# Optimization experiments

Hardware: AMD Instinct MI355X
Metric: run time of the kernel (lower is better)

Reference implementation:

```python
import jax, jax.numpy as jnp
import numpy as np

B, S, I, H, O = 2048, 128, 1, 512, 1
OUT_SEQ_LEN = 24


def setup_inputs() -> dict:
    key = jax.random.key(0)
    ks = jax.random.split(key, 12)
    s = 1.0 / np.sqrt(H)
    u = lambda k, shape: jax.random.uniform(k, shape, jnp.float32, -s, s)
    return {
        'x': jax.random.normal(ks[0], (B, S, I), jnp.float32),
        'enc_Wih': u(ks[1], (H, I)),
        'enc_Whh': u(ks[2], (H, H)),
        'enc_bih': u(ks[3], (H,)),
        'enc_bhh': u(ks[4], (H,)),
        'dec_Wih': u(ks[5], (H, I)),
        'dec_Whh': u(ks[6], (H, H)),
        'dec_bih': u(ks[7], (H,)),
        'dec_bhh': u(ks[8], (H,)),
        'fc_W': u(ks[9], (O, H)),
        'fc_b': u(ks[10], (O,)),
    }


def reference(x, enc_Wih, enc_Whh, enc_bih, enc_bhh,
              dec_Wih, dec_Whh, dec_bih, dec_bhh, fc_W, fc_b):
    batch = x.shape[0]
    h0 = jnp.zeros((batch, H), x.dtype)

    # Encoder: vanilla tanh RNN, h_t = tanh(x_t W_ih^T + b_ih + h_{t-1} W_hh^T + b_hh)
    def enc_step(h, xt):
        h2 = jnp.tanh(xt @ enc_Wih.T + enc_bih + h @ enc_Whh.T + enc_bhh)
        return h2, None

    hT, _ = jax.lax.scan(enc_step, h0, jnp.swapaxes(x, 0, 1))  # scan over S

    def dec_step(carry, _):
        h, inp = carry
        h2 = jnp.tanh(inp @ dec_Wih.T + dec_bih + h @ dec_Whh.T + dec_bhh)
        out = h2 @ fc_W.T + fc_b  # [B, O]
        return (h2, out), out

    dec_in0 = x[:, -1, :]  # [B, I]
    _, outs = jax.lax.scan(dec_step, (hT, dec_in0), None, length=OUT_SEQ_LEN)
    outputs = jnp.swapaxes(outs, 0, 1)  # [B, OUT_SEQ_LEN, O]
    return outputs[..., 0]  # squeeze(-1) since O == 1
```

## Files before the change

### kernel.cpp

```cpp
#include <hip/hip_runtime.h>
#include <math.h>

#define BATCH 2048
#define SEQ   128
#define HID   512
#define OUTT  24
#define RPB   8
#define NBLK  (BATCH/RPB)
#define TPB   512
#define NTW   4
#define KTN   (HID/32)
#define HOLD_KT 8
#define LDSB_KT 3
#define STR_KT  (KTN - HOLD_KT - LDSB_KT)
#define LDSB_BASE HOLD_KT
#define STR_BASE  (HOLD_KT + LDSB_KT)

typedef _Float16 half8 __attribute__((ext_vector_type(8)));
typedef float   floatx4 __attribute__((ext_vector_type(4)));

__device__ __forceinline__ float ftanh(float x) {
    float e = __builtin_amdgcn_exp2f(x * 2.885390081777927f);
    float r = __builtin_amdgcn_rcpf(e + 1.0f);
    return fmaf(-2.0f, r, 1.0f);
}

__global__ __launch_bounds__(256) void pack_wfrag(const float* __restrict__ W,
                                                  _Float16* __restrict__ Bw)
{
    int id   = blockIdx.x * 256 + threadIdx.x;
    int lane = id & 63;
    int nt   = (id >> 6) & 31;
    int kt   = id >> 11;
    int n  = nt * 16 + (lane & 15);
    int k0 = kt * 32 + (lane >> 4) * 8;
    const float* src = W + (size_t)n * HID + k0;
    half8 v;
    #pragma unroll
    for (int j = 0; j < 8; j++) v[j] = (_Float16)src[j];
    *(half8*)&Bw[(size_t)id * 8] = v;
}

__global__ __launch_bounds__(TPB, 2) void rnn_persist(
    const float* __restrict__ x,
    const _Float16* __restrict__ BwE,
    const _Float16* __restrict__ BwD,
    const float* __restrict__ encWih, const float* __restrict__ encBih,
    const float* __restrict__ encBhh,
    const float* __restrict__ decWih, const float* __restrict__ decBih,
    const float* __restrict__ decBhh,
    const float* __restrict__ fcW, const float* __restrict__ fcB,
    float* __restrict__ out)
{
    __shared__ _Float16 A[2][KTN * 512];
    __shared__ _Float16 BwL[LDSB_KT * 16384];
    __shared__ float    xs[RPB][SEQ];
    __shared__ float    dec_in_s[RPB];

    const int tid  = threadIdx.x;
    const int lane = tid & 63;
    const int wv   = tid >> 6;
    const int row0 = blockIdx.x * RPB;
    const int c    = lane & 15;
    const int q    = lane >> 4;
    const int qh   = q & 1;
    const int lohalf = q >> 1;
    const int mB   = qh * 4;

    float eWi[NTW], eBb[NTW], dWi[NTW], dBb[NTW];
    #pragma unroll
    for (int i = 0; i < NTW; i++) {
        int n = (wv * NTW + i) * 16 + c;
        eWi[i] = encWih[n]; eBb[i] = encBih[n] + encBhh[n];
        dWi[i] = decWih[n]; dBb[i] = decBih[n] + decBhh[n];
    }
    const float fcb0 = fcB[0];

    {
        const float4* xg = (const float4*)(x + (size_t)row0 * SEQ);
        if (tid < RPB * SEQ / 4) ((float4*)xs)[tid] = xg[tid];
    }

    for (int i = tid; i < KTN * 512 / 2; i += TPB) ((int*)A[0])[i] = 0;

    {
        const float4* src = (const float4*)(BwE + (size_t)LDSB_BASE * 16384);
        float4* dst = (float4*)BwL;
        #pragma unroll
        for (int i = 0; i < LDSB_KT * 16384 / 8 / TPB; i++)
            dst[i * TPB + tid] = src[i * TPB + tid];
    }

    const int    ldsAoff = q * 128 + ((c ^ q) << 3);
    const size_t bbase   = (size_t)(wv * NTW) * 512 + (size_t)lane * 8;
    const int    bbL     = wv * NTW * 512 + lane * 8;

    half8 wreg[HOLD_KT][NTW];
    #pragma unroll
    for (int kt = 0; kt < HOLD_KT; kt++)
        #pragma unroll
        for (int i = 0; i < NTW; i++)
            wreg[kt][i] = *(const half8*)&BwE[bbase + (size_t)kt * 16384 + i * 512];

    __syncthreads();

    int cur = 0;
    for (int t = 0; t < SEQ + OUTT; t++) {
        const bool enc = (t < SEQ);
        const _Float16* __restrict__ Bw = enc ? BwE : BwD;
        const _Float16* Ac = A[cur];

        if (t == SEQ) {
            #pragma unroll
            for (int kt = 0; kt < HOLD_KT; kt++)
                #pragma unroll
                for (int i = 0; i < NTW; i++)
                    wreg[kt][i] = *(const half8*)&BwD[bbase + (size_t)kt * 16384 + i * 512];
            const float4* src = (const float4*)(BwD + (size_t)LDSB_BASE * 16384);
            float4* dst = (float4*)BwL;
            #pragma unroll
            for (int i = 0; i < LDSB_KT * 16384 / 8 / TPB; i++)
                dst[i * TPB + tid] = src[i * TPB + tid];
            __syncthreads();
        }

        #pragma unroll
        for (int kt = 0; kt < HOLD_KT; kt++)
            #pragma unroll
            for (int i = 0; i < NTW; i++)
                asm volatile("" : "+v"(wreg[kt][i]));

        floatx4 acc[NTW];
        #pragma unroll
        for (int i = 0; i < NTW; i++) acc[i] = (floatx4){0.f, 0.f, 0.f, 0.f};

        half8 bcur[NTW], bnxt[NTW];
        #pragma unroll
        for (int i = 0; i < NTW; i++) {
            bcur[i] = *(const half8*)&Bw[bbase + (size_t)STR_BASE * 16384 + i * 512];
            bnxt[i] = *(const half8*)&Bw[bbase + (size_t)(STR_BASE + 1) * 16384 + i * 512];
        }

        #pragma unroll
        for (int kt = 0; kt < HOLD_KT; kt++) {
            half8 a = *(const half8*)&Ac[kt * 512 + ldsAoff];
            #pragma unroll
            for (int i = 0; i < NTW; i++)
                acc[i] = __builtin_amdgcn_mfma_f32_16x16x32_f16(a, wreg[kt][i], acc[i], 0, 0, 0);
        }

        #pragma unroll
        for (int kl = 0; kl < LDSB_KT; kl++) {
            half8 a = *(const half8*)&Ac[(LDSB_BASE + kl) * 512 + ldsAoff];
            #pragma unroll
            for (int i = 0; i < NTW; i++) {
                half8 b = *(const half8*)&BwL[kl * 16384 + bbL + i * 512];
                acc[i] = __builtin_amdgcn_mfma_f32_16x16x32_f16(a, b, acc[i], 0, 0, 0);
            }
        }

        #pragma unroll
        for (int s = 0; s < STR_KT; s++) {
            const int kt = STR_BASE + s;
            half8 bpre[NTW];
            if (s + 2 < STR_KT) {
                #pragma unroll
                for (int i = 0; i < NTW; i++)
                    bpre[i] = *(const half8*)&Bw[bbase + (size_t)(kt + 2) * 16384 + i * 512];
            }
            half8 a = *(const half8*)&Ac[kt * 512 + ldsAoff];
            #pragma unroll
            for (int i = 0; i < NTW; i++)
                acc[i] = __builtin_amdgcn_mfma_f32_16x16x32_f16(a, bcur[i], acc[i], 0, 0, 0);
            #pragma unroll
            for (int i = 0; i < NTW; i++) {
                bcur[i] = bnxt[i];
                if (s + 2 < STR_KT) bnxt[i] = bpre[i];
            }
        }

        float inp[4];
        if (enc) {
            #pragma unroll
            for (int r = 0; r < 4; r++) inp[r] = xs[mB + r][t];
        } else if (t == SEQ) {
            #pragma unroll
            for (int r = 0; r < 4; r++) inp[r] = xs[mB + r][SEQ - 1];
        } else {
            #pragma unroll
            for (int r = 0; r < 4; r++) inp[r] = dec_in_s[mB + r];
        }

        const int nxt = cur ^ 1;
        #pragma unroll
        for (int i = 0; i < NTW; i++) {
            int n = (wv * NTW + i) * 16 + c;
            int G = (n >> 3) & 3;
            int base = (n >> 5) * 512 + G * 128 + (n & 7);
            float wi = enc ? eWi[i] : dWi[i];
            float bb = enc ? eBb[i] : dBb[i];
            #pragma unroll
            for (int r = 0; r < 4; r++) {
                float sum = acc[i][r] + __shfl_xor(acc[i][r], 32, 64);
                float v = ftanh(sum + inp[r] * wi + bb);
                _Float16 hh = (_Float16)v;
                _Float16 rs = (_Float16)(v - (float)hh);
                int mw = mB + r + (lohalf << 3);
                A[nxt][base + ((mw ^ G) << 3)] = lohalf ? rs : hh;
            }
        }
        __syncthreads();

        if (!enc) {
            const int m = wv;
            float sfc = 0.f;
            #pragma unroll
            for (int ii = 0; ii < HID / 64; ii++) {
                int k = ii * 64 + lane;
                int G = (k >> 3) & 3;
                int a0 = (k >> 5) * 512 + G * 128 + (k & 7);
                float hv = (float)A[nxt][a0 + ((m ^ G) << 3)]
                         + (float)A[nxt][a0 + (((m + 8) ^ G) << 3)];
                sfc = fmaf(hv, fcW[k], sfc);
            }
            #pragma unroll
            for (int off = 32; off > 0; off >>= 1)
                sfc += __shfl_down(sfc, off, 64);
            if (lane == 0) {
                float o = sfc + fcb0;
                dec_in_s[m] = o;
                out[(size_t)(row0 + m) * OUTT + (t - SEQ)] = o;
            }
            __syncthreads();
        }
        cur = nxt;
    }
}

extern "C" void kernel_launch(void* const* d_in, const int* in_sizes, int n_in,
                              void* d_out, int out_size, void* d_ws, size_t ws_size,
                              hipStream_t stream)
{
    const float* x        = (const float*)d_in[0];
    const float* enc_Wih  = (const float*)d_in[1];
    const float* enc_Whh  = (const float*)d_in[2];
    const float* enc_bih  = (const float*)d_in[3];
    const float* enc_bhh  = (const float*)d_in[4];
    const float* dec_Wih  = (const float*)d_in[5];
    const float* dec_Whh  = (const float*)d_in[6];
    const float* dec_bih  = (const float*)d_in[7];
    const float* dec_bhh  = (const float*)d_in[8];
    const float* fc_W     = (const float*)d_in[9];
    const float* fc_b     = (const float*)d_in[10];
    float* out = (float*)d_out;

    const size_t wfrag = (size_t)HID * HID;
    _Float16* BwE = (_Float16*)d_ws;
    _Float16* BwD = BwE + wfrag;

    pack_wfrag<<<HID * HID / (256 * 8), 256, 0, stream>>>(enc_Whh, BwE);
    pack_wfrag<<<HID * HID / (256 * 8), 256, 0, stream>>>(dec_Whh, BwD);

    rnn_persist<<<NBLK, TPB, 0, stream>>>(
        x, BwE, BwD,
        enc_Wih, enc_bih, enc_bhh,
        dec_Wih, dec_bih, dec_bhh,
        fc_W, fc_b, out);
}
```

Before: 658.3 us.

## Single-buffer hidden state, shift weight split from registers to LDS

Replaces the double-buffered hidden-state LDS tile with a single buffer. An extra barrier after the MFMA loop keeps the buffer from being overwritten while other waves still read it. It also moves the weight split from 8 register-held K tiles plus 3 LDS tiles to 6 register tiles plus 4 LDS tiles, using the LDS space the single buffer frees. The asm register pin is dropped and volatile loads are used instead. This is meant to cut register pressure and streamed global traffic, at the cost of one more block-wide sync per timestep.

```diff
diff --git a/kernel.cpp b/kernel.cpp
--- a/kernel.cpp
+++ b/kernel.cpp
@@ -10,8 +10,8 @@
 #define TPB   512
 #define NTW   4
 #define KTN   (HID/32)
-#define HOLD_KT 8
-#define LDSB_KT 3
+#define HOLD_KT 6
+#define LDSB_KT 4
 #define STR_KT  (KTN - HOLD_KT - LDSB_KT)
 #define LDSB_BASE HOLD_KT
 #define STR_BASE  (HOLD_KT + LDSB_KT)
@@ -52,7 +52,7 @@
     const float* __restrict__ fcW, const float* __restrict__ fcB,
     float* __restrict__ out)
 {
-    __shared__ _Float16 A[2][KTN * 512];
+    __shared__ _Float16 A[KTN * 512];
     __shared__ _Float16 BwL[LDSB_KT * 16384];
     __shared__ float    xs[RPB][SEQ];
     __shared__ float    dec_in_s[RPB];
@@ -81,7 +81,7 @@
         if (tid < RPB * SEQ / 4) ((float4*)xs)[tid] = xg[tid];
     }
 
-    for (int i = tid; i < KTN * 512 / 2; i += TPB) ((int*)A[0])[i] = 0;
+    for (int i = tid; i < KTN * 512 / 2; i += TPB) ((int*)A)[i] = 0;
 
     {
         const float4* src = (const float4*)(BwE + (size_t)LDSB_BASE * 16384);
@@ -100,22 +100,20 @@
     for (int kt = 0; kt < HOLD_KT; kt++)
         #pragma unroll
         for (int i = 0; i < NTW; i++)
-            wreg[kt][i] = *(const half8*)&BwE[bbase + (size_t)kt * 16384 + i * 512];
+            wreg[kt][i] = *(const volatile half8*)&BwE[bbase + (size_t)kt * 16384 + i * 512];
 
     __syncthreads();
 
-    int cur = 0;
     for (int t = 0; t < SEQ + OUTT; t++) {
         const bool enc = (t < SEQ);
         const _Float16* __restrict__ Bw = enc ? BwE : BwD;
-        const _Float16* Ac = A[cur];
 
         if (t == SEQ) {
             #pragma unroll
             for (int kt = 0; kt < HOLD_KT; kt++)
                 #pragma unroll
                 for (int i = 0; i < NTW; i++)
-                    wreg[kt][i] = *(const half8*)&BwD[bbase + (size_t)kt * 16384 + i * 512];
+                    wreg[kt][i] = *(const volatile half8*)&BwD[bbase + (size_t)kt * 16384 + i * 512];
             const float4* src = (const float4*)(BwD + (size_t)LDSB_BASE * 16384);
             float4* dst = (float4*)BwL;
             #pragma unroll
@@ -124,12 +122,6 @@
             __syncthreads();
         }
 
-        #pragma unroll
-        for (int kt = 0; kt < HOLD_KT; kt++)
-            #pragma unroll
-            for (int i = 0; i < NTW; i++)
-                asm volatile("" : "+v"(wreg[kt][i]));
-
         floatx4 acc[NTW];
         #pragma unroll
         for (int i = 0; i < NTW; i++) acc[i] = (floatx4){0.f, 0.f, 0.f, 0.f};
@@ -143,7 +135,7 @@
 
         #pragma unroll
         for (int kt = 0; kt < HOLD_KT; kt++) {
-            half8 a = *(const half8*)&Ac[kt * 512 + ldsAoff];
+            half8 a = *(const half8*)&A[kt * 512 + ldsAoff];
             #pragma unroll
             for (int i = 0; i < NTW; i++)
                 acc[i] = __builtin_amdgcn_mfma_f32_16x16x32_f16(a, wreg[kt][i], acc[i], 0, 0, 0);
@@ -151,7 +143,7 @@
 
         #pragma unroll
         for (int kl = 0; kl < LDSB_KT; kl++) {
-            half8 a = *(const half8*)&Ac[(LDSB_BASE + kl) * 512 + ldsAoff];
+            half8 a = *(const half8*)&A[(LDSB_BASE + kl) * 512 + ldsAoff];
             #pragma unroll
             for (int i = 0; i < NTW; i++) {
                 half8 b = *(const half8*)&BwL[kl * 16384 + bbL + i * 512];
@@ -168,7 +160,7 @@
                 for (int i = 0; i < NTW; i++)
                     bpre[i] = *(const half8*)&Bw[bbase + (size_t)(kt + 2) * 16384 + i * 512];
             }
-            half8 a = *(const half8*)&Ac[kt * 512 + ldsAoff];
+            half8 a = *(const half8*)&A[kt * 512 + ldsAoff];
             #pragma unroll
             for (int i = 0; i < NTW; i++)
                 acc[i] = __builtin_amdgcn_mfma_f32_16x16x32_f16(a, bcur[i], acc[i], 0, 0, 0);
@@ -179,6 +171,8 @@
             }
         }
 
+        __syncthreads();
+
         float inp[4];
         if (enc) {
             #pragma unroll
@@ -191,7 +185,6 @@
             for (int r = 0; r < 4; r++) inp[r] = dec_in_s[mB + r];
         }
 
-        const int nxt = cur ^ 1;
         #pragma unroll
         for (int i = 0; i < NTW; i++) {
             int n = (wv * NTW + i) * 16 + c;
@@ -206,7 +199,7 @@
                 _Float16 hh = (_Float16)v;
                 _Float16 rs = (_Float16)(v - (float)hh);
                 int mw = mB + r + (lohalf << 3);
-                A[nxt][base + ((mw ^ G) << 3)] = lohalf ? rs : hh;
+                A[base + ((mw ^ G) << 3)] = lohalf ? rs : hh;
             }
         }
         __syncthreads();
@@ -219,8 +212,8 @@
                 int k = ii * 64 + lane;
                 int G = (k >> 3) & 3;
                 int a0 = (k >> 5) * 512 + G * 128 + (k & 7);
-                float hv = (float)A[nxt][a0 + ((m ^ G) << 3)]
-                         + (float)A[nxt][a0 + (((m + 8) ^ G) << 3)];
+                float hv = (float)A[a0 + ((m ^ G) << 3)]
+                         + (float)A[a0 + (((m + 8) ^ G) << 3)];
                 sfc = fmaf(hv, fcW[k], sfc);
             }
             #pragma unroll
@@ -233,7 +226,6 @@
             }
             __syncthreads();
         }
-        cur = nxt;
     }
 }
 
```

Result: slower. 681.5 us (+3.5%).
